# Kernel optimization log

Measured on AMD Instinct MI355X. Metric: run time of the kernel, lower is better.

## Reference

```python
import jax, jax.numpy as jnp
import numpy as np

B, N, D, H = 2, 2048, 1024, 16
HD = D // H

def setup_inputs() -> dict:
    key = jax.random.key(0)
    ks = jax.random.split(key, 8)
    s = lambda fan_in: 1.0 / np.sqrt(fan_in)
    return {
        "x": jax.random.normal(ks[0], (B, N, D), jnp.float32),
        "coverage": jax.random.uniform(ks[1], (B, N, 1), jnp.float32),
        "w_qkv": jax.random.normal(ks[2], (D, 3 * D), jnp.float32) * s(D),
        "w_out": jax.random.normal(ks[3], (D, D), jnp.float32) * s(D),
        "b_out": jnp.zeros((D,), jnp.float32),
        "w_ce1": jax.random.normal(ks[4], (1, D // 4), jnp.float32),
        "b_ce1": jnp.zeros((D // 4,), jnp.float32),
        "w_ce2": jax.random.normal(ks[5], (D // 4, H), jnp.float32) * s(D // 4),
        "b_ce2": jnp.zeros((H,), jnp.float32),
        "w_fg1": jax.random.normal(ks[6], (D, D // 4), jnp.float32) * s(D),
        "b_fg1": jnp.zeros((D // 4,), jnp.float32),
        "w_fg2": jax.random.normal(ks[7], (D // 4, 1), jnp.float32) * s(D // 4),
        "b_fg2": jnp.zeros((1,), jnp.float32),
    }

def reference(x, coverage, w_qkv, w_out, b_out, w_ce1, b_ce1, w_ce2, b_ce2,
              w_fg1, b_fg1, w_fg2, b_fg2):
    b, n, d = x.shape
    h = w_ce2.shape[1]
    hd = d // h
    scale = hd ** -0.5
    qkv = x @ w_qkv  # (B,N,3D)
    q, k, v = jnp.split(qkv, 3, axis=-1)
    q = q.reshape(b, n, h, hd).transpose(0, 2, 1, 3)  # (B,H,N,hd)
    k = k.reshape(b, n, h, hd).transpose(0, 2, 1, 3)
    v = v.reshape(b, n, h, hd).transpose(0, 2, 1, 3)
    attn = jnp.einsum("bhnd,bhmd->bhnm", q, k) * scale  # (B,H,N,N)
    # coverage bias: MLP(1 -> D/4 -> H), broadcast over query dim
    cov = jax.nn.silu(coverage @ w_ce1 + b_ce1) @ w_ce2 + b_ce2  # (B,N,H)
    cov_bias = cov.transpose(0, 2, 1)[:, :, None, :]  # (B,H,1,N)
    # fusion gate on mean-pooled features
    x_pooled = x.mean(axis=1)  # (B,D)
    g = jax.nn.sigmoid(jax.nn.silu(x_pooled @ w_fg1 + b_fg1) @ w_fg2 + b_fg2)  # (B,1)
    g = g[:, :, None, None]  # (B,1,1,1)
    # g*(attn+bias) + (1-g)*attn == attn + g*bias (exact same math)
    attn = attn + g * cov_bias
    attn = jax.nn.softmax(attn, axis=-1)
    out = jnp.einsum("bhnm,bhmd->bhnd", attn, v)  # (B,H,N,hd)
    out = out.transpose(0, 2, 1, 3).reshape(b, n, d)
    return out @ w_out + b_out
```

## Files before the change

kernel.cpp:

```cpp
#include <hip/hip_runtime.h>
#include <math.h>

typedef __bf16 bf16_t;
typedef __bf16 bf16x8 __attribute__((ext_vector_type(8)));
typedef __bf16 bf16x4 __attribute__((ext_vector_type(4)));
typedef float f32x4 __attribute__((ext_vector_type(4)));

#define MFMA16(a, b, c) __builtin_amdgcn_mfma_f32_16x16x32_bf16((a), (b), (c), 0, 0, 0)

constexpr int Bc = 2, Nc = 2048, Dc = 1024, Hc = 16, HDc = 64;
constexpr float C1 = 0.18033688011112042f;
constexpr float LOG2E = 1.4426950408889634f;

__device__ __forceinline__ void glds16(const bf16_t* g, bf16_t* l) {
    __builtin_amdgcn_global_load_lds(
        (const __attribute__((address_space(1))) unsigned int*)g,
        (__attribute__((address_space(3))) unsigned int*)l, 16, 0, 0);
}

__device__ __forceinline__ void glds4(const float* g, float* l) {
    __builtin_amdgcn_global_load_lds(
        (const __attribute__((address_space(1))) unsigned int*)g,
        (__attribute__((address_space(3))) unsigned int*)l, 4, 0, 0);
}

__device__ __forceinline__ void tr64_body(const float* __restrict__ src,
                                          bf16_t* __restrict__ dst, int R, int C,
                                          int bx, int by, bf16_t* tile, int t) {
    int r0 = by * 64, c0 = bx * 64;
    int cl = t & 63, rl = t >> 6;
#pragma unroll
    for (int p = 0; p < 16; ++p) {
        int r = p * 4 + rl;
        tile[r * 66 + cl] = (bf16_t)src[(size_t)(r0 + r) * C + c0 + cl];
    }
    __syncthreads();
#pragma unroll
    for (int p = 0; p < 16; ++p) {
        int r = p * 4 + rl;
        dst[(size_t)(c0 + r) * R + r0 + cl] = tile[cl * 66 + r];
    }
}

__global__ __launch_bounds__(256) void prep(const float* __restrict__ x,
                                            bf16_t* __restrict__ Xb,
                                            const float* __restrict__ w_qkv,
                                            bf16_t* __restrict__ Wt,
                                            const float* __restrict__ w_out,
                                            bf16_t* __restrict__ WoT,
                                            float* __restrict__ pooled,
                                            const float* __restrict__ coverage,
                                            const float* __restrict__ w_ce1,
                                            const float* __restrict__ b_ce1,
                                            const float* __restrict__ w_ce2,
                                            const float* __restrict__ b_ce2,
                                            float* __restrict__ cbias) {
    __shared__ bf16_t tile[64 * 66];
    int bid = blockIdx.x, t = threadIdx.x;
    if (bid < 4096) {
        int i = (bid * 256 + t) * 4;
        float4 v = *(const float4*)(x + i);
        bf16x4 o = { (bf16_t)v.x, (bf16_t)v.y, (bf16_t)v.z, (bf16_t)v.w };
        *(bf16x4*)(Xb + i) = o;
    } else if (bid < 4864) {
        int bb = bid - 4096;
        tr64_body(w_qkv, Wt, 1024, 3072, bb % 48, bb / 48, tile, t);
    } else if (bid < 5120) {
        int bb = bid - 4864;
        tr64_body(w_out, WoT, 1024, 1024, bb & 15, bb >> 4, tile, t);
    } else if (bid < 5376) {
        int blk = bid - 5120;
        int b = blk >> 7, ch = blk & 127;
        int c = t * 4;
        float s0 = 0.f, s1 = 0.f, s2 = 0.f, s3 = 0.f;
        for (int rr = 0; rr < 16; ++rr) {
            float4 v = *(const float4*)(x + (size_t)(b * Nc + ch * 16 + rr) * Dc + c);
            s0 += v.x; s1 += v.y; s2 += v.z; s3 += v.w;
        }
        atomicAdd(&pooled[b * Dc + c + 0], s0);
        atomicAdd(&pooled[b * Dc + c + 1], s1);
        atomicAdd(&pooled[b * Dc + c + 2], s2);
        atomicAdd(&pooled[b * Dc + c + 3], s3);
    } else {
        int blk = bid - 5376;
        int h = t & 15;
        int gn = blk * 16 + (t >> 4);
        int b = gn >> 11, n = gn & 2047;
        float c = coverage[gn];
        float acc = b_ce2[h];
        for (int j = 0; j < 256; ++j) {
            float tv = c * w_ce1[j] + b_ce1[j];
            tv = tv / (1.0f + __expf(-tv));
            acc += tv * w_ce2[j * 16 + h];
        }
        cbias[((size_t)b * 16 + h) * 2048 + n] = LOG2E * acc;
    }
}

__global__ __launch_bounds__(256) void qkv_gemm(const bf16_t* __restrict__ Xb,
                                                const bf16_t* __restrict__ Wt,
                                                bf16_t* __restrict__ Q,
                                                bf16_t* __restrict__ Kb,
                                                bf16_t* __restrict__ Vt,
                                                const float* __restrict__ pooled,
                                                const float* __restrict__ w_fg1,
                                                const float* __restrict__ b_fg1,
                                                const float* __restrict__ w_fg2,
                                                float* __restrict__ hacc) {
    __shared__ __align__(16) bf16_t At[128 * 32];
    __shared__ __align__(16) bf16_t Bt[128 * 32];
    int t = threadIdx.x;

    if (blockIdx.y == 24) {
        __shared__ float red[4];
        int blk = blockIdx.x;
        int b = blk >> 4, jb = (blk & 15) * 16;
        for (int jj = 0; jj < 16; ++jj) {
            int j = jb + jj;
            float p = 0.f;
#pragma unroll
            for (int i = 0; i < 4; ++i) {
                int d = t * 4 + i;
                p += pooled[b * 1024 + d] * w_fg1[d * 256 + j];
            }
#pragma unroll
            for (int off = 32; off > 0; off >>= 1) p += __shfl_down(p, off);
            if ((t & 63) == 0) red[t >> 6] = p;
            __syncthreads();
            if (t == 0) {
                float hj = (red[0] + red[1] + red[2] + red[3]) * (1.0f / 2048.0f) + b_fg1[j];
                hj = hj / (1.0f + __expf(-hj));
                atomicAdd(&hacc[b], hj * w_fg2[j]);
            }
            __syncthreads();
        }
        return;
    }

    int w = t >> 6, lane = t & 63;
    int l16 = lane & 15, quad = lane >> 4;
    int wm = w & 1, wx = w >> 1;
    int m0 = blockIdx.x * 128;
    int n0 = blockIdx.y * 128;
    f32x4 acc[4][4] = {};
    int sw = (l16 >> 2) & 3;

    for (int k0 = 0; k0 < 1024; k0 += 32) {
#pragma unroll
        for (int i = 0; i < 2; ++i) {
            int fb = i * 4096 + w * 1024;
            int f = fb + lane * 16;
            int row = f >> 6;
            int ch = (f >> 4) & 3;
            int sc = ch ^ ((row >> 2) & 3);
            glds16(Wt + (size_t)(n0 + row) * 1024 + k0 + sc * 8, At + (fb >> 1));
            glds16(Xb + (size_t)(m0 + row) * 1024 + k0 + sc * 8, Bt + (fb >> 1));
        }
        __syncthreads();
        bf16x8 afr[4], bfr[4];
#pragma unroll
        for (int mi = 0; mi < 4; ++mi)
            afr[mi] = *(const bf16x8*)(At + (wm * 64 + mi * 16 + l16) * 32 + ((quad ^ sw) * 8));
#pragma unroll
        for (int ni = 0; ni < 4; ++ni)
            bfr[ni] = *(const bf16x8*)(Bt + (wx * 64 + ni * 16 + l16) * 32 + ((quad ^ sw) * 8));
#pragma unroll
        for (int mi = 0; mi < 4; ++mi)
#pragma unroll
            for (int ni = 0; ni < 4; ++ni)
                acc[mi][ni] = MFMA16(afr[mi], bfr[ni], acc[mi][ni]);
        __syncthreads();
    }

    int sec = n0 >> 10;
    float scq = (sec == 0) ? C1 : 1.0f;
#pragma unroll
    for (int mi = 0; mi < 4; ++mi) {
        int gc = n0 + wm * 64 + mi * 16 + quad * 4;
        int dcol = gc & 1023;
        int h = dcol >> 6, hd = dcol & 63;
#pragma unroll
        for (int ni = 0; ni < 4; ++ni) {
            int gx = m0 + wx * 64 + ni * 16 + l16;
            int b = gx >> 11, n = gx & 2047;
            size_t bh = (size_t)(b * 16 + h);
            if (sec == 2) {
#pragma unroll
                for (int r = 0; r < 4; ++r)
                    Vt[(bh * 64 + hd + r) * 2048 + n] = (bf16_t)acc[mi][ni][r];
            } else {
                bf16x4 pk = { (bf16_t)(acc[mi][ni][0] * scq), (bf16_t)(acc[mi][ni][1] * scq),
                              (bf16_t)(acc[mi][ni][2] * scq), (bf16_t)(acc[mi][ni][3] * scq) };
                bf16_t* dst = (sec == 0 ? Q : Kb);
                *(bf16x4*)(dst + (bh * 2048 + n) * 64 + hd) = pk;
            }
        }
    }
}

__global__ __launch_bounds__(128) void attn_k(const bf16_t* __restrict__ Q,
                                              const bf16_t* __restrict__ Kb,
                                              const bf16_t* __restrict__ Vt,
                                              const float* __restrict__ cbias,
                                              const float* __restrict__ hacc,
                                              const float* __restrict__ b_fg2,
                                              bf16_t* __restrict__ O) {
    __shared__ __align__(16) bf16_t kbuf[2][64 * 64];
    __shared__ __align__(16) bf16_t vbuf[2][64 * 64];
    __shared__ __align__(16) float bbias[2][64];
    int t = threadIdx.x, w = t >> 6, lane = t & 63;
    int l16 = lane & 15, quad = lane >> 4;
    int bh = blockIdx.y;
    int b = bh >> 4, h = bh & 15;
    int qa = blockIdx.x * 64 + w * 32;
    const bf16_t* Qh = Q + (size_t)bh * 2048 * 64;
    const bf16_t* Kh = Kb + (size_t)bh * 2048 * 64;
    const bf16_t* Vh = Vt + (size_t)bh * 64 * 2048;
    const float* bih = cbias + (size_t)bh * 2048;
    float g = 1.0f / (1.0f + __expf(-(hacc[b] + b_fg2[0])));

    int krow[4], ksc[4];
#pragma unroll
    for (int c = 0; c < 4; ++c) {
        int f = w * 4096 + c * 1024 + lane * 16;
        int row = f >> 7, ch = (f >> 4) & 7;
        krow[c] = row;
        ksc[c] = ch ^ (row & 7);
    }

    bf16x8 qf[2][2];
#pragma unroll
    for (int qt = 0; qt < 2; ++qt)
#pragma unroll
        for (int dh = 0; dh < 2; ++dh)
            qf[qt][dh] = *(const bf16x8*)(Qh + (size_t)(qa + qt * 16 + l16) * 64 + dh * 32 + quad * 8);

    f32x4 o[2][4] = {};
    f32x4 lacc[2] = {};
    bf16x8 onesb;
#pragma unroll
    for (int i = 0; i < 8; ++i) onesb[i] = (bf16_t)1.0f;
    int swl = l16 & 7;
    int qh = quad >> 1, ql = quad & 1;

    int bk0 = l16 * 64 + ((quad ^ swl) * 8);
    int bk1 = l16 * 64 + (((4 + quad) ^ swl) * 8);
    int bv0 = l16 * 64 + ql * 4 + ((qh ^ swl) * 8);
    int bv1 = l16 * 64 + ql * 4 + (((2 + qh) ^ swl) * 8);
    int bv2 = l16 * 64 + ql * 4 + (((4 + qh) ^ swl) * 8);
    int bv3 = l16 * 64 + ql * 4 + (((6 + qh) ^ swl) * 8);

    auto stage = [&](int tile_, int bf) {
        int jn = tile_ * 64;
        bf16_t* kd = &kbuf[bf][w * 2048];
        bf16_t* vd = &vbuf[bf][w * 2048];
#pragma unroll
        for (int c = 0; c < 4; ++c)
            glds16(Kh + (size_t)(jn + krow[c]) * 64 + ksc[c] * 8, kd + c * 512);
#pragma unroll
        for (int c = 0; c < 4; ++c)
            glds16(Vh + (size_t)krow[c] * 2048 + jn + ksc[c] * 8, vd + c * 512);
        glds4(bih + jn + lane, &bbias[bf][0]);
    };

    stage(0, 0);

    for (int it = 0; it < 32; ++it) {
        int sel = it & 1;
        asm volatile("s_waitcnt lgkmcnt(0)" ::: "memory");
        __builtin_amdgcn_s_barrier();
        if (it + 1 < 32) {
            stage(it + 1, sel ^ 1);
            asm volatile("s_waitcnt vmcnt(9)" ::: "memory");
        } else {
            asm volatile("s_waitcnt vmcnt(0)" ::: "memory");
        }
        __builtin_amdgcn_s_barrier();
        __builtin_amdgcn_sched_barrier(0);

        const bf16_t* kb = &kbuf[sel][0];
        const bf16_t* vb = &vbuf[sel][0];
        const float* bp = &bbias[sel][0];

        f32x4 s[2][4];
        __builtin_amdgcn_s_setprio(1);
#pragma unroll
        for (int kt = 0; kt < 4; ++kt) {
            f32x4 bv = *(const f32x4*)(bp + kt * 16 + quad * 4);
            f32x4 bi = { bv[0] * g, bv[1] * g, bv[2] * g, bv[3] * g };
            bf16x8 kf0 = *(const bf16x8*)(kb + kt * 1024 + bk0);
            bf16x8 kf1 = *(const bf16x8*)(kb + kt * 1024 + bk1);
#pragma unroll
            for (int qt = 0; qt < 2; ++qt) {
                s[qt][kt] = MFMA16(kf0, qf[qt][0], bi);
                s[qt][kt] = MFMA16(kf1, qf[qt][1], s[qt][kt]);
            }
        }
        __builtin_amdgcn_s_setprio(0);

        bf16x8 pf[2][2];
#pragma unroll
        for (int qt = 0; qt < 2; ++qt) {
#pragma unroll
            for (int kt = 0; kt < 4; ++kt)
#pragma unroll
                for (int r = 0; r < 4; ++r)
                    s[qt][kt][r] = __builtin_amdgcn_exp2f(s[qt][kt][r]);
#pragma unroll
            for (int pv = 0; pv < 2; ++pv) {
                bf16x8 tmp;
#pragma unroll
                for (int i = 0; i < 4; ++i) {
                    tmp[i]     = (bf16_t)s[qt][2 * pv][i];
                    tmp[i + 4] = (bf16_t)s[qt][2 * pv + 1][i];
                }
                pf[qt][pv] = tmp;
            }
        }

        __builtin_amdgcn_s_setprio(1);
#pragma unroll
        for (int qt = 0; qt < 2; ++qt) {
            lacc[qt] = MFMA16(pf[qt][0], onesb, lacc[qt]);
            lacc[qt] = MFMA16(pf[qt][1], onesb, lacc[qt]);
        }
#pragma unroll
        for (int dt = 0; dt < 4; ++dt) {
            bf16x4 va0 = *(const bf16x4*)(vb + dt * 1024 + bv0);
            bf16x4 vc0 = *(const bf16x4*)(vb + dt * 1024 + bv1);
            bf16x8 vf0 = __builtin_shufflevector(va0, vc0, 0, 1, 2, 3, 4, 5, 6, 7);
            bf16x4 va1 = *(const bf16x4*)(vb + dt * 1024 + bv2);
            bf16x4 vc1 = *(const bf16x4*)(vb + dt * 1024 + bv3);
            bf16x8 vf1 = __builtin_shufflevector(va1, vc1, 0, 1, 2, 3, 4, 5, 6, 7);
#pragma unroll
            for (int qt = 0; qt < 2; ++qt) {
                o[qt][dt] = MFMA16(pf[qt][0], vf0, o[qt][dt]);
                o[qt][dt] = MFMA16(pf[qt][1], vf1, o[qt][dt]);
            }
        }
        __builtin_amdgcn_s_setprio(0);
    }

#pragma unroll
    for (int qt = 0; qt < 2; ++qt) {
        f32x4 rinv;
#pragma unroll
        for (int r = 0; r < 4; ++r) rinv[r] = 1.0f / lacc[qt][r];
#pragma unroll
        for (int dt = 0; dt < 4; ++dt)
#pragma unroll
            for (int r = 0; r < 4; ++r) {
                int row = qa + qt * 16 + quad * 4 + r;
                O[(size_t)(b * 2048 + row) * 1024 + h * 64 + dt * 16 + l16] =
                    (bf16_t)(o[qt][dt][r] * rinv[r]);
            }
    }
}

__global__ __launch_bounds__(256) void out_gemm(const bf16_t* __restrict__ A,
                                                const bf16_t* __restrict__ Wt,
                                                const float* __restrict__ bias,
                                                float* __restrict__ Cout) {
    __shared__ __align__(16) bf16_t At[128 * 32];
    __shared__ __align__(16) bf16_t Bt[128 * 32];
    int t = threadIdx.x, w = t >> 6, lane = t & 63;
    int l16 = lane & 15, quad = lane >> 4;
    int wm = w & 1, wx = w >> 1;
    int m0 = blockIdx.x * 128;
    int n0 = blockIdx.y * 128;
    f32x4 acc[4][4] = {};
    int sw = (l16 >> 2) & 3;

    for (int k0 = 0; k0 < 1024; k0 += 32) {
#pragma unroll
        for (int i = 0; i < 2; ++i) {
            int fb = i * 4096 + w * 1024;
            int f = fb + lane * 16;
            int row = f >> 6;
            int ch = (f >> 4) & 3;
            int sc = ch ^ ((row >> 2) & 3);
            glds16(Wt + (size_t)(n0 + row) * 1024 + k0 + sc * 8, At + (fb >> 1));
            glds16(A + (size_t)(m0 + row) * 1024 + k0 + sc * 8, Bt + (fb >> 1));
        }
        __syncthreads();
        bf16x8 afr[4], bfr[4];
#pragma unroll
        for (int mi = 0; mi < 4; ++mi)
            afr[mi] = *(const bf16x8*)(At + (wm * 64 + mi * 16 + l16) * 32 + ((quad ^ sw) * 8));
#pragma unroll
        for (int ni = 0; ni < 4; ++ni)
            bfr[ni] = *(const bf16x8*)(Bt + (wx * 64 + ni * 16 + l16) * 32 + ((quad ^ sw) * 8));
#pragma unroll
        for (int mi = 0; mi < 4; ++mi)
#pragma unroll
            for (int ni = 0; ni < 4; ++ni)
                acc[mi][ni] = MFMA16(afr[mi], bfr[ni], acc[mi][ni]);
        __syncthreads();
    }

#pragma unroll
    for (int mi = 0; mi < 4; ++mi) {
        int gc = n0 + wm * 64 + mi * 16 + quad * 4;
        float4 bv = *(const float4*)(bias + gc);
#pragma unroll
        for (int ni = 0; ni < 4; ++ni) {
            int gx = m0 + wx * 64 + ni * 16 + l16;
            float4 ov = { acc[mi][ni][0] + bv.x, acc[mi][ni][1] + bv.y,
                          acc[mi][ni][2] + bv.z, acc[mi][ni][3] + bv.w };
            *(float4*)(Cout + (size_t)gx * 1024 + gc) = ov;
        }
    }
}

extern "C" void kernel_launch(void* const* d_in, const int* in_sizes, int n_in,
                              void* d_out, int out_size, void* d_ws, size_t ws_size,
                              hipStream_t stream) {
    const float* x     = (const float*)d_in[0];
    const float* cov   = (const float*)d_in[1];
    const float* w_qkv = (const float*)d_in[2];
    const float* w_out = (const float*)d_in[3];
    const float* b_out = (const float*)d_in[4];
    const float* w_ce1 = (const float*)d_in[5];
    const float* b_ce1 = (const float*)d_in[6];
    const float* w_ce2 = (const float*)d_in[7];
    const float* b_ce2 = (const float*)d_in[8];
    const float* w_fg1 = (const float*)d_in[9];
    const float* b_fg1 = (const float*)d_in[10];
    const float* w_fg2 = (const float*)d_in[11];
    const float* b_fg2 = (const float*)d_in[12];

    char* ws = (char*)d_ws;
    bf16_t* Wt     = (bf16_t*)(ws);
    bf16_t* WoT    = (bf16_t*)(ws + 6291456);
    bf16_t* Xb     = (bf16_t*)(ws + 8388608);
    bf16_t* Qb     = (bf16_t*)(ws + 16777216);
    bf16_t* Kbb    = (bf16_t*)(ws + 25165824);
    bf16_t* Vt     = (bf16_t*)(ws + 33554432);
    bf16_t* Ob     = (bf16_t*)(ws + 41943040);
    float*  pooled = (float*)(ws + 50331648);
    float*  hacc   = (float*)(ws + 50339840);
    float*  biasb  = (float*)(ws + 50340096);

    hipMemsetAsync(pooled, 0, 8200, stream);
    prep<<<5632, 256, 0, stream>>>(x, Xb, w_qkv, Wt, w_out, WoT, pooled,
                                   cov, w_ce1, b_ce1, w_ce2, b_ce2, biasb);
    qkv_gemm<<<dim3(32, 25), 256, 0, stream>>>(Xb, Wt, Qb, Kbb, Vt,
                                               pooled, w_fg1, b_fg1, w_fg2, hacc);
    attn_k<<<dim3(32, 32), 128, 0, stream>>>(Qb, Kbb, Vt, biasb, hacc, b_fg2, Ob);
    out_gemm<<<dim3(32, 8), 256, 0, stream>>>(Ob, WoT, b_out, (float*)d_out);
}
```

Baseline: 267.1 us.

## Share K/V tiles across four waves in attention and restructure prep kernel

The attention kernel now runs 256 threads (4 waves) per block covering 128 queries, so each staged K/V tile in LDS is reused by twice as many query rows. Each wave issues half as many async loads, and the vmcnt wait threshold is adjusted to match. The prep kernel reorders its work so the coverage-bias MLP goes first, staging the weights in shared memory and splitting the reduction over waves instead of redoing per-thread global loops. The x-to-bf16 conversion now handles four chunks per block. Fewer attention blocks (512) may lower latency hiding, and the changed vmcnt count must stay correct for the pipeline.

```diff
diff --git a/kernel.cpp b/kernel.cpp
--- a/kernel.cpp
+++ b/kernel.cpp
@@ -55,21 +55,50 @@
                                             const float* __restrict__ w_ce2,
                                             const float* __restrict__ b_ce2,
                                             float* __restrict__ cbias) {
-    __shared__ bf16_t tile[64 * 66];
+    __shared__ __align__(16) float smem[8768];
     int bid = blockIdx.x, t = threadIdx.x;
-    if (bid < 4096) {
-        int i = (bid * 256 + t) * 4;
-        float4 v = *(const float4*)(x + i);
-        bf16x4 o = { (bf16_t)v.x, (bf16_t)v.y, (bf16_t)v.z, (bf16_t)v.w };
-        *(bf16x4*)(Xb + i) = o;
-    } else if (bid < 4864) {
-        int bb = bid - 4096;
-        tr64_body(w_qkv, Wt, 1024, 3072, bb % 48, bb / 48, tile, t);
-    } else if (bid < 5120) {
-        int bb = bid - 4864;
-        tr64_body(w_out, WoT, 1024, 1024, bb & 15, bb >> 4, tile, t);
-    } else if (bid < 5376) {
-        int blk = bid - 5120;
+
+    if (bid < 64) {
+        float* w1s = smem;
+        float* b1s = smem + 256;
+        float* w2s = smem + 512;
+        float* part = smem + 4608;
+        int b = bid >> 5, n0 = (bid & 31) * 64;
+        w1s[t] = w_ce1[t];
+        b1s[t] = b_ce1[t];
+        {
+            float4* w2v = (float4*)w2s;
+            const float4* g4 = (const float4*)w_ce2;
+#pragma unroll
+            for (int i = 0; i < 4; ++i) w2v[i * 256 + t] = g4[i * 256 + t];
+        }
+        __syncthreads();
+        int wv = t >> 6, lane2 = t & 63;
+        float c = coverage[b * 2048 + n0 + lane2];
+        float acc[16];
+#pragma unroll
+        for (int hh = 0; hh < 16; ++hh) acc[hh] = 0.f;
+        for (int jj = 0; jj < 64; ++jj) {
+            int j = wv * 64 + jj;
+            float tv = fmaf(c, w1s[j], b1s[j]);
+            tv = tv / (1.0f + __expf(-tv));
+#pragma unroll
+            for (int hh = 0; hh < 16; ++hh)
+                acc[hh] = fmaf(tv, w2s[j * 16 + hh], acc[hh]);
+        }
+#pragma unroll
+        for (int hh = 0; hh < 16; ++hh) part[lane2 * 65 + wv * 16 + hh] = acc[hh];
+        __syncthreads();
+#pragma unroll
+        for (int i = 0; i < 4; ++i) {
+            int idx = t + i * 256;
+            int nl = idx >> 4, hh = idx & 15;
+            const float* pr = part + nl * 65 + hh;
+            float s = pr[0] + pr[16] + pr[32] + pr[48];
+            cbias[((size_t)b * 16 + hh) * 2048 + n0 + nl] = LOG2E * (s + b_ce2[hh]);
+        }
+    } else if (bid < 320) {
+        int blk = bid - 64;
         int b = blk >> 7, ch = blk & 127;
         int c = t * 4;
         float s0 = 0.f, s1 = 0.f, s2 = 0.f, s3 = 0.f;
@@ -81,19 +110,21 @@
         atomicAdd(&pooled[b * Dc + c + 1], s1);
         atomicAdd(&pooled[b * Dc + c + 2], s2);
         atomicAdd(&pooled[b * Dc + c + 3], s3);
+    } else if (bid < 1088) {
+        int bb = bid - 320;
+        tr64_body(w_qkv, Wt, 1024, 3072, bb % 48, bb / 48, (bf16_t*)smem, t);
+    } else if (bid < 1344) {
+        int bb = bid - 1088;
+        tr64_body(w_out, WoT, 1024, 1024, bb & 15, bb >> 4, (bf16_t*)smem, t);
     } else {
-        int blk = bid - 5376;
-        int h = t & 15;
-        int gn = blk * 16 + (t >> 4);
-        int b = gn >> 11, n = gn & 2047;
-        float c = coverage[gn];
-        float acc = b_ce2[h];
-        for (int j = 0; j < 256; ++j) {
-            float tv = c * w_ce1[j] + b_ce1[j];
-            tv = tv / (1.0f + __expf(-tv));
-            acc += tv * w_ce2[j * 16 + h];
-        }
-        cbias[((size_t)b * 16 + h) * 2048 + n] = LOG2E * acc;
+        int base = (bid - 1344) * 4096 + t * 4;
+#pragma unroll
+        for (int c = 0; c < 4; ++c) {
+            int i = base + c * 1024;
+            float4 v = *(const float4*)(x + i);
+            bf16x4 o = { (bf16_t)v.x, (bf16_t)v.y, (bf16_t)v.z, (bf16_t)v.w };
+            *(bf16x4*)(Xb + i) = o;
+        }
     }
 }
 
@@ -198,7 +229,7 @@
     }
 }
 
-__global__ __launch_bounds__(128) void attn_k(const bf16_t* __restrict__ Q,
+__global__ __launch_bounds__(256) void attn_k(const bf16_t* __restrict__ Q,
                                               const bf16_t* __restrict__ Kb,
                                               const bf16_t* __restrict__ Vt,
                                               const float* __restrict__ cbias,
@@ -212,21 +243,17 @@
     int l16 = lane & 15, quad = lane >> 4;
     int bh = blockIdx.y;
     int b = bh >> 4, h = bh & 15;
-    int qa = blockIdx.x * 64 + w * 32;
+    int qa = blockIdx.x * 128 + w * 32;
     const bf16_t* Qh = Q + (size_t)bh * 2048 * 64;
     const bf16_t* Kh = Kb + (size_t)bh * 2048 * 64;
     const bf16_t* Vh = Vt + (size_t)bh * 64 * 2048;
     const float* bih = cbias + (size_t)bh * 2048;
     float g = 1.0f / (1.0f + __expf(-(hacc[b] + b_fg2[0])));
 
-    int krow[4], ksc[4];
-#pragma unroll
-    for (int c = 0; c < 4; ++c) {
-        int f = w * 4096 + c * 1024 + lane * 16;
-        int row = f >> 7, ch = (f >> 4) & 7;
-        krow[c] = row;
-        ksc[c] = ch ^ (row & 7);
-    }
+    int fb0 = w * 2048, fb1 = fb0 + 1024;
+    int f0 = fb0 + lane * 16, f1 = fb1 + lane * 16;
+    int krow0 = f0 >> 7, kch0 = ((f0 >> 4) & 7) ^ (krow0 & 7);
+    int krow1 = f1 >> 7, kch1 = ((f1 >> 4) & 7) ^ (krow1 & 7);
 
     bf16x8 qf[2][2];
 #pragma unroll
@@ -252,14 +279,10 @@
 
     auto stage = [&](int tile_, int bf) {
         int jn = tile_ * 64;
-        bf16_t* kd = &kbuf[bf][w * 2048];
-        bf16_t* vd = &vbuf[bf][w * 2048];
-#pragma unroll
-        for (int c = 0; c < 4; ++c)
-            glds16(Kh + (size_t)(jn + krow[c]) * 64 + ksc[c] * 8, kd + c * 512);
-#pragma unroll
-        for (int c = 0; c < 4; ++c)
-            glds16(Vh + (size_t)krow[c] * 2048 + jn + ksc[c] * 8, vd + c * 512);
+        glds16(Kh + (size_t)(jn + krow0) * 64 + kch0 * 8, &kbuf[bf][fb0 >> 1]);
+        glds16(Kh + (size_t)(jn + krow1) * 64 + kch1 * 8, &kbuf[bf][fb1 >> 1]);
+        glds16(Vh + (size_t)krow0 * 2048 + jn + kch0 * 8, &vbuf[bf][fb0 >> 1]);
+        glds16(Vh + (size_t)krow1 * 2048 + jn + kch1 * 8, &vbuf[bf][fb1 >> 1]);
         glds4(bih + jn + lane, &bbias[bf][0]);
     };
 
@@ -271,7 +294,7 @@
         __builtin_amdgcn_s_barrier();
         if (it + 1 < 32) {
             stage(it + 1, sel ^ 1);
-            asm volatile("s_waitcnt vmcnt(9)" ::: "memory");
+            asm volatile("s_waitcnt vmcnt(5)" ::: "memory");
         } else {
             asm volatile("s_waitcnt vmcnt(0)" ::: "memory");
         }
@@ -442,10 +465,10 @@
     float*  biasb  = (float*)(ws + 50340096);
 
     hipMemsetAsync(pooled, 0, 8200, stream);
-    prep<<<5632, 256, 0, stream>>>(x, Xb, w_qkv, Wt, w_out, WoT, pooled,
+    prep<<<2368, 256, 0, stream>>>(x, Xb, w_qkv, Wt, w_out, WoT, pooled,
                                    cov, w_ce1, b_ce1, w_ce2, b_ce2, biasb);
     qkv_gemm<<<dim3(32, 25), 256, 0, stream>>>(Xb, Wt, Qb, Kbb, Vt,
                                                pooled, w_fg1, b_fg1, w_fg2, hacc);
-    attn_k<<<dim3(32, 32), 128, 0, stream>>>(Qb, Kbb, Vt, biasb, hacc, b_fg2, Ob);
+    attn_k<<<dim3(16, 32), 256, 0, stream>>>(Qb, Kbb, Vt, biasb, hacc, b_fg2, Ob);
     out_gemm<<<dim3(32, 8), 256, 0, stream>>>(Ob, WoT, b_out, (float*)d_out);
 }
```

Result: faster. 240.3 us (-10.0%).
